# Optimization experiments

Hardware: AMD Instinct MI355X
Metric: run time of the kernel (lower is better)

Reference implementation:

```python
import jax, jax.numpy as jnp
import numpy as np

B, H, W, K, A = 4096, 32, 32, 20, 4


def setup_inputs() -> dict:
    key = jax.random.key(0)
    k_wall, k_agent, k_goal, k_phi, k_l1, k_l2 = jax.random.split(key, 6)
    # obs channels: 0 = wall/feature map (random), 1 = one-hot agent pos, 2 = one-hot goal pos
    walls = jax.random.uniform(k_wall, (B, H, W), dtype=jnp.float32)
    agent_idx = jax.random.randint(k_agent, (B,), 0, H * W)
    goal_idx = jax.random.randint(k_goal, (B,), 0, H * W)
    agent = jax.nn.one_hot(agent_idx, H * W, dtype=jnp.float32).reshape(B, H, W)
    goal = jax.nn.one_hot(goal_idx, H * W, dtype=jnp.float32).reshape(B, H, W)
    obs = jnp.stack([walls, agent, goal], axis=-1)  # (B,H,W,3)
    obs_flat = obs.reshape(B, H * W * 3)
    din = H * W * 3
    return {
        "obs_flat": obs_flat,
        "Phi_w": jax.random.normal(k_phi, (din, 2 * H * W), dtype=jnp.float32) * 0.02,
        "Phi_b": jnp.zeros((2 * H * W,), jnp.float32),
        "L1_w": jax.random.normal(k_l1, (36, 16), dtype=jnp.float32) * 0.1,
        "L1_b": jnp.zeros((16,), jnp.float32),
        "L2_w": jax.random.normal(k_l2, (16, A), dtype=jnp.float32) * 0.1,
        "L2_b": jnp.zeros((A,), jnp.float32),
    }


def _mvprop(r, p):
    # K-step value propagation: V <- max(V, r + p*(best 4-neighbor V - r))
    # p = sigmoid(...) >= 0, so max over the 4 shifted nv values equals nv of the max shift.
    def body(V, _):
        pv = jnp.pad(V, ((0, 0), (1, 1), (1, 1)))
        nbr = jnp.maximum(
            jnp.maximum(pv[:, :-2, 1:-1], pv[:, 2:, 1:-1]),   # up, down
            jnp.maximum(pv[:, 1:-1, :-2], pv[:, 1:-1, 2:]),   # left, right
        )
        return jnp.maximum(V, r + p * (nbr - r)), None
    V, _ = jax.lax.scan(body, r, None, length=K)
    return V


def reference(obs_flat, Phi_w, Phi_b, L1_w, L1_b, L2_w, L2_b):
    b = obs_flat.shape[0]
    obs = obs_flat.reshape(b, H, W, 3)
    phi = jax.nn.sigmoid(obs_flat @ Phi_w + Phi_b).reshape(b, H, W, 2)
    r, p = phi[..., 0], phi[..., 1]
    V = _mvprop(r, p)  # (b,H,W)
    obs_val = jnp.concatenate([obs, V[..., None]], axis=-1)  # (b,H,W,4)
    padded = jnp.pad(obs_val, ((0, 0), (1, 1), (1, 1), (0, 0)))
    # agent position: exactly one nonzero in channel 1 per sample -> argmax
    idx = jnp.argmax(obs[..., 1].reshape(b, -1), axis=1)
    pi, pj = idx // W, idx % W
    # 3x3 neighborhood around agent in padded grid (start = pos+1-1 = pos)
    def slice_one(ov, i, j):
        return jax.lax.dynamic_slice(ov, (i, j, 0), (3, 3, 4))
    sel = jax.vmap(slice_one)(padded, pi, pj)  # (b,3,3,4)
    h = jax.nn.relu(sel.reshape(b, 36) @ L1_w + L1_b)
    logit = h @ L2_w + L2_b
    return logit
```

## Files before the change

### kernel.cpp

```cpp
#include <hip/hip_runtime.h>
#include <hip/hip_fp16.h>

#define BATCH 4096
#define HH 32
#define WW 32
#define KPROP 20
#define NACT 4
#define DIN 3072
#define DPHI 2048
#define HWC 1024
#define KC 1024

typedef _Float16 h8_t __attribute__((ext_vector_type(8)));
typedef _Float16 h4_t __attribute__((ext_vector_type(4)));
typedef float f32x4 __attribute__((ext_vector_type(4)));

__device__ inline float sigmoidf(float x) { return 1.0f / (1.0f + __expf(-x)); }

__device__ inline float dpp_shr1(float x) {
    return __int_as_float(__builtin_amdgcn_update_dpp(
        0, __float_as_int(x), 0x111, 0xF, 0xF, true));
}
__device__ inline float dpp_shl1(float x) {
    return __int_as_float(__builtin_amdgcn_update_dpp(
        0, __float_as_int(x), 0x101, 0xF, 0xF, true));
}

__global__ __launch_bounds__(256) void prep_fused_kernel(
    const float* __restrict__ obs,
    const float* __restrict__ Phi_w,
    _Float16* __restrict__ W16,
    _Float16* __restrict__ PwT,
    _Float16* __restrict__ Pag,
    int* __restrict__ aidx, int* __restrict__ gidx)
{
    __shared__ float tile[32][33];
    if (blockIdx.x < BATCH) {
        const int t = blockIdx.x * 256 + threadIdx.x;
        const int b = t >> 8;
        const int c0 = (t & 255) * 4;
        const float* src = obs + (size_t)b * DIN + 3 * c0;
        const float4 f0 = *(const float4*)(src);
        const float4 f1 = *(const float4*)(src + 4);
        const float4 f2 = *(const float4*)(src + 8);
        h4_t w;
        w[0] = (_Float16)f0.x; w[1] = (_Float16)f0.w;
        w[2] = (_Float16)f1.z; w[3] = (_Float16)f2.y;
        *(h4_t*)(W16 + (size_t)b * KC + c0) = w;
        if (f0.y > 0.5f) aidx[b] = c0;
        if (f1.x > 0.5f) aidx[b] = c0 + 1;
        if (f1.w > 0.5f) aidx[b] = c0 + 2;
        if (f2.z > 0.5f) aidx[b] = c0 + 3;
        if (f0.z > 0.5f) gidx[b] = c0;
        if (f1.y > 0.5f) gidx[b] = c0 + 1;
        if (f2.x > 0.5f) gidx[b] = c0 + 2;
        if (f2.w > 0.5f) gidx[b] = c0 + 3;
    } else {
        const int bid = blockIdx.x - BATCH;
        const int ni = bid & 63;
        const int ci = bid >> 6;
        const int tx = threadIdx.x & 31;
        const int ty = threadIdx.x >> 5;
        #pragma unroll
        for (int s = 0; s < 4; s++) {
            const int r = ty + 8 * s;
            const int c = ci * 32 + r;
            const int n = ni * 32 + tx;
            tile[r][tx] = Phi_w[(size_t)(3 * c) * DPHI + n];
            Pag[(size_t)c * DPHI + n]         = (_Float16)Phi_w[(size_t)(3 * c + 1) * DPHI + n];
            Pag[(size_t)(HWC + c) * DPHI + n] = (_Float16)Phi_w[(size_t)(3 * c + 2) * DPHI + n];
        }
        __syncthreads();
        #pragma unroll
        for (int s = 0; s < 4; s++) {
            const int r = ty + 8 * s;
            PwT[(size_t)(ni * 32 + r) * KC + ci * 32 + tx] = (_Float16)tile[tx][r];
        }
    }
}

__global__ __launch_bounds__(256) void gemm_pre_kernel(
    const _Float16* __restrict__ A,
    const _Float16* __restrict__ Bt,
    const float* __restrict__ bias,
    _Float16* __restrict__ pre)
{
    const int tid  = threadIdx.x;
    const int lane = tid & 63;
    const int wid  = tid >> 6;
    const int m0 = blockIdx.y * 64;
    const int n0 = blockIdx.x * 256 + wid * 64;
    const int lm = lane & 15;
    const int kq = lane >> 4;

    const _Float16* Ap = A  + (size_t)(m0 + lm) * KC + kq * 8;
    const _Float16* Bp = Bt + (size_t)(n0 + lm) * KC + kq * 8;

    f32x4 acc[4][4] = {};
    h8_t a_cur[4], b_cur[4], a_nxt[4], b_nxt[4];

    #pragma unroll
    for (int i = 0; i < 4; i++) {
        a_cur[i] = *(const h8_t*)(Ap + (size_t)i * 16 * KC);
        b_cur[i] = *(const h8_t*)(Bp + (size_t)i * 16 * KC);
    }

    for (int k0 = 32; k0 <= KC; k0 += 32) {
        if (k0 < KC) {
            #pragma unroll
            for (int i = 0; i < 4; i++) {
                a_nxt[i] = *(const h8_t*)(Ap + (size_t)i * 16 * KC + k0);
                b_nxt[i] = *(const h8_t*)(Bp + (size_t)i * 16 * KC + k0);
            }
        }
        #pragma unroll
        for (int mt = 0; mt < 4; mt++)
            #pragma unroll
            for (int nt = 0; nt < 4; nt++)
                acc[mt][nt] = __builtin_amdgcn_mfma_f32_16x16x32_f16(
                    a_cur[mt], b_cur[nt], acc[mt][nt], 0, 0, 0);
        #pragma unroll
        for (int i = 0; i < 4; i++) { a_cur[i] = a_nxt[i]; b_cur[i] = b_nxt[i]; }
    }

    #pragma unroll
    for (int nt = 0; nt < 4; nt++) {
        const int col = n0 + nt * 16 + lm;
        const float bcol = bias[col];
        #pragma unroll
        for (int mt = 0; mt < 4; mt++) {
            #pragma unroll
            for (int r = 0; r < 4; r++) {
                const int row = m0 + mt * 16 + kq * 4 + r;
                pre[(size_t)row * DPHI + col] = (_Float16)(acc[mt][nt][r] + bcol);
            }
        }
    }
}

__global__ __launch_bounds__(256, 4) void vprop_head_kernel(
    const _Float16* __restrict__ pre,
    const _Float16* __restrict__ Pag,
    const float* __restrict__ obs,
    const int* __restrict__ aidx,
    const int* __restrict__ gidx,
    const float* __restrict__ L1w,
    const float* __restrict__ L1b,
    const float* __restrict__ L2w,
    const float* __restrict__ L2b,
    float* __restrict__ out)
{
    __shared__ __align__(16) float Vg[4][HWC];
    __shared__ float sel[4][36], hbuf[4][16];

    const int tid  = threadIdx.x;
    const int w    = tid >> 6;
    const int lane = tid & 63;
    const int b    = blockIdx.x * 4 + w;
    const int bi   = lane & 15;
    const int bj   = lane >> 4;
    const int ai = aidx[b];
    const int gi = gidx[b];

    const _Float16* pb = pre + (size_t)b * DPHI;
    const _Float16* ra = Pag + (size_t)ai * DPHI;
    const _Float16* rg = Pag + (size_t)(HWC + gi) * DPHI;

    float v[2][8], p[2][8], a[2][8];
    #pragma unroll
    for (int r = 0; r < 2; r++) {
        const int off = 64 * (2 * bi + r) + 16 * bj;
        const h8_t ph0 = *(const h8_t*)(pb + off), ph1 = *(const h8_t*)(pb + off + 8);
        const h8_t pa0 = *(const h8_t*)(ra + off), pa1 = *(const h8_t*)(ra + off + 8);
        const h8_t pg0 = *(const h8_t*)(rg + off), pg1 = *(const h8_t*)(rg + off + 8);
        #pragma unroll
        for (int c = 0; c < 4; c++) {
            const float rv = sigmoidf((float)ph0[2*c]   + (float)pa0[2*c]   + (float)pg0[2*c]);
            const float pv = sigmoidf((float)ph0[2*c+1] + (float)pa0[2*c+1] + (float)pg0[2*c+1]);
            v[r][c] = rv; p[r][c] = pv; a[r][c] = rv * (1.0f - pv);
            const float rv2 = sigmoidf((float)ph1[2*c]   + (float)pa1[2*c]   + (float)pg1[2*c]);
            const float pv2 = sigmoidf((float)ph1[2*c+1] + (float)pa1[2*c+1] + (float)pg1[2*c+1]);
            v[r][c+4] = rv2; p[r][c+4] = pv2; a[r][c+4] = rv2 * (1.0f - pv2);
        }
    }

    for (int it = 0; it < KPROP; it++) {
        float uh[8], dh[8], lh[2], rh[2];
        #pragma unroll
        for (int c = 0; c < 8; c++) {
            uh[c] = dpp_shr1(v[1][c]);
            dh[c] = dpp_shl1(v[0][c]);
        }
        #pragma unroll
        for (int r = 0; r < 2; r++) {
            lh[r] = __shfl(v[r][7], lane - 16);
            rh[r] = __shfl(v[r][0], lane + 16);
            if (bj == 0) lh[r] = 0.0f;
            if (bj == 3) rh[r] = 0.0f;
        }
        float nb[2][8];
        #pragma unroll
        for (int c = 0; c < 8; c++) {
            const float lf0 = (c == 0) ? lh[0] : v[0][c-1];
            const float rt0 = (c == 7) ? rh[0] : v[0][c+1];
            const float lf1 = (c == 0) ? lh[1] : v[1][c-1];
            const float rt1 = (c == 7) ? rh[1] : v[1][c+1];
            nb[0][c] = fmaxf(fmaxf(uh[c], v[1][c]), fmaxf(lf0, rt0));
            nb[1][c] = fmaxf(fmaxf(v[0][c], dh[c]), fmaxf(lf1, rt1));
        }
        #pragma unroll
        for (int r = 0; r < 2; r++)
            #pragma unroll
            for (int c = 0; c < 8; c++)
                v[r][c] = fmaxf(v[r][c], fmaf(p[r][c], nb[r][c], a[r][c]));
    }

    #pragma unroll
    for (int r = 0; r < 2; r++) {
        float4 lo, hi;
        lo.x = v[r][0]; lo.y = v[r][1]; lo.z = v[r][2]; lo.w = v[r][3];
        hi.x = v[r][4]; hi.y = v[r][5]; hi.z = v[r][6]; hi.w = v[r][7];
        const int base = (2 * bi + r) * 32 + 8 * bj;
        *(float4*)&Vg[w][base]     = lo;
        *(float4*)&Vg[w][base + 4] = hi;
    }
    __syncthreads();

    const int pi = ai >> 5, pj = ai & 31;
    if (lane < 36) {
        const int cell = lane >> 2;
        const int ch = lane & 3;
        const int di = pi + cell / 3 - 1;
        const int dj = pj + cell % 3 - 1;
        float vv = 0.0f;
        if (di >= 0 && di < HH && dj >= 0 && dj < WW) {
            const int c = di * WW + dj;
            vv = (ch < 3) ? obs[(size_t)b * DIN + 3 * c + ch] : Vg[w][c];
        }
        sel[w][lane] = vv;
    }
    __syncthreads();

    if (lane < 16) {
        float h = L1b[lane];
        #pragma unroll
        for (int k = 0; k < 36; k++) h += sel[w][k] * L1w[k * 16 + lane];
        hbuf[w][lane] = fmaxf(h, 0.0f);
    }
    __syncthreads();

    if (lane < 4) {
        float o = L2b[lane];
        #pragma unroll
        for (int t = 0; t < 16; t++) o += hbuf[w][t] * L2w[t * 4 + lane];
        out[(size_t)b * NACT + lane] = o;
    }
}

extern "C" void kernel_launch(void* const* d_in, const int* in_sizes, int n_in,
                              void* d_out, int out_size, void* d_ws, size_t ws_size,
                              hipStream_t stream) {
    const float* obs   = (const float*)d_in[0];
    const float* Phi_w = (const float*)d_in[1];
    const float* Phi_b = (const float*)d_in[2];
    const float* L1w   = (const float*)d_in[3];
    const float* L1b   = (const float*)d_in[4];
    const float* L2w   = (const float*)d_in[5];
    const float* L2b   = (const float*)d_in[6];
    float* out = (float*)d_out;

    char* ws = (char*)d_ws;
    _Float16* pre = (_Float16*)ws;
    _Float16* W16 = (_Float16*)(ws + 16777216);
    _Float16* PwT = (_Float16*)(ws + 25165824);
    _Float16* Pag = (_Float16*)(ws + 29360128);
    int* aidx = (int*)(ws + 37748736);
    int* gidx = aidx + BATCH;

    prep_fused_kernel<<<BATCH + 2048, 256, 0, stream>>>(obs, Phi_w, W16, PwT, Pag, aidx, gidx);
    gemm_pre_kernel<<<dim3(DPHI / 256, BATCH / 64), 256, 0, stream>>>(W16, PwT, Phi_b, pre);
    vprop_head_kernel<<<BATCH / 4, 256, 0, stream>>>(pre, Pag, obs, aidx, gidx,
                                                     L1w, L1b, L2w, L2b, out);
}
```

Baseline: 197.2 us.

## Pre-pack GEMM operands into MFMA fragment layout with double-buffered loads

The prep kernel now writes the fp16 A and B operands into a tiled layout where each 16-row by 8-k fragment is contiguous. Each wave can then fetch a whole MFMA fragment with one fully coalesced 1 KB load instead of 16 strided row segments. The GEMM main loop is restructured into two register buffers that alternate each half-iteration to overlap loads with MFMAs. The LDS transpose of Phi_w is removed, so B is written with scattered 2-byte stores, which may make the prep stage more expensive.

```diff
diff --git a/kernel.cpp b/kernel.cpp
--- a/kernel.cpp
+++ b/kernel.cpp
@@ -10,6 +10,7 @@
 #define DPHI 2048
 #define HWC 1024
 #define KC 1024
+#define TILE_ELEMS (16 * KC)
 
 typedef _Float16 h8_t __attribute__((ext_vector_type(8)));
 typedef _Float16 h4_t __attribute__((ext_vector_type(4)));
@@ -26,15 +27,18 @@
         0, __float_as_int(x), 0x101, 0xF, 0xF, true));
 }
 
+__device__ inline size_t pack_off(int row, int k) {
+    return (size_t)(row >> 4) * TILE_ELEMS + (k >> 3) * 128 + (row & 15) * 8 + (k & 7);
+}
+
 __global__ __launch_bounds__(256) void prep_fused_kernel(
     const float* __restrict__ obs,
     const float* __restrict__ Phi_w,
-    _Float16* __restrict__ W16,
-    _Float16* __restrict__ PwT,
+    _Float16* __restrict__ A_pack,
+    _Float16* __restrict__ B_pack,
     _Float16* __restrict__ Pag,
     int* __restrict__ aidx, int* __restrict__ gidx)
 {
-    __shared__ float tile[32][33];
     if (blockIdx.x < BATCH) {
         const int t = blockIdx.x * 256 + threadIdx.x;
         const int b = t >> 8;
@@ -46,7 +50,7 @@
         h4_t w;
         w[0] = (_Float16)f0.x; w[1] = (_Float16)f0.w;
         w[2] = (_Float16)f1.z; w[3] = (_Float16)f2.y;
-        *(h4_t*)(W16 + (size_t)b * KC + c0) = w;
+        *(h4_t*)(A_pack + pack_off(b, c0)) = w;
         if (f0.y > 0.5f) aidx[b] = c0;
         if (f1.x > 0.5f) aidx[b] = c0 + 1;
         if (f1.w > 0.5f) aidx[b] = c0 + 2;
@@ -66,22 +70,17 @@
             const int r = ty + 8 * s;
             const int c = ci * 32 + r;
             const int n = ni * 32 + tx;
-            tile[r][tx] = Phi_w[(size_t)(3 * c) * DPHI + n];
+            const float w0 = Phi_w[(size_t)(3 * c) * DPHI + n];
             Pag[(size_t)c * DPHI + n]         = (_Float16)Phi_w[(size_t)(3 * c + 1) * DPHI + n];
             Pag[(size_t)(HWC + c) * DPHI + n] = (_Float16)Phi_w[(size_t)(3 * c + 2) * DPHI + n];
-        }
-        __syncthreads();
-        #pragma unroll
-        for (int s = 0; s < 4; s++) {
-            const int r = ty + 8 * s;
-            PwT[(size_t)(ni * 32 + r) * KC + ci * 32 + tx] = (_Float16)tile[tx][r];
+            B_pack[pack_off(n, c)] = (_Float16)w0;
         }
     }
 }
 
 __global__ __launch_bounds__(256) void gemm_pre_kernel(
-    const _Float16* __restrict__ A,
-    const _Float16* __restrict__ Bt,
+    const _Float16* __restrict__ A_pack,
+    const _Float16* __restrict__ B_pack,
     const float* __restrict__ bias,
     _Float16* __restrict__ pre)
 {
@@ -93,34 +92,47 @@
     const int lm = lane & 15;
     const int kq = lane >> 4;
 
-    const _Float16* Ap = A  + (size_t)(m0 + lm) * KC + kq * 8;
-    const _Float16* Bp = Bt + (size_t)(n0 + lm) * KC + kq * 8;
+    const _Float16* Abase = A_pack + (size_t)(blockIdx.y * 4) * TILE_ELEMS + 8 * lane;
+    const _Float16* Bbase = B_pack + (size_t)(blockIdx.x * 16 + wid * 4) * TILE_ELEMS + 8 * lane;
 
     f32x4 acc[4][4] = {};
-    h8_t a_cur[4], b_cur[4], a_nxt[4], b_nxt[4];
+    h8_t a0[4], b0[4], a1[4], b1[4];
 
     #pragma unroll
     for (int i = 0; i < 4; i++) {
-        a_cur[i] = *(const h8_t*)(Ap + (size_t)i * 16 * KC);
-        b_cur[i] = *(const h8_t*)(Bp + (size_t)i * 16 * KC);
-    }
-
-    for (int k0 = 32; k0 <= KC; k0 += 32) {
-        if (k0 < KC) {
-            #pragma unroll
-            for (int i = 0; i < 4; i++) {
-                a_nxt[i] = *(const h8_t*)(Ap + (size_t)i * 16 * KC + k0);
-                b_nxt[i] = *(const h8_t*)(Bp + (size_t)i * 16 * KC + k0);
-            }
-        }
+        a0[i] = *(const h8_t*)(Abase + i * TILE_ELEMS);
+        b0[i] = *(const h8_t*)(Bbase + i * TILE_ELEMS);
+        a1[i] = *(const h8_t*)(Abase + i * TILE_ELEMS + 32 * 16);
+        b1[i] = *(const h8_t*)(Bbase + i * TILE_ELEMS + 32 * 16);
+    }
+
+    for (int k0 = 0; k0 < KC; k0 += 64) {
         #pragma unroll
         for (int mt = 0; mt < 4; mt++)
             #pragma unroll
             for (int nt = 0; nt < 4; nt++)
                 acc[mt][nt] = __builtin_amdgcn_mfma_f32_16x16x32_f16(
-                    a_cur[mt], b_cur[nt], acc[mt][nt], 0, 0, 0);
-        #pragma unroll
-        for (int i = 0; i < 4; i++) { a_cur[i] = a_nxt[i]; b_cur[i] = b_nxt[i]; }
+                    a0[mt], b0[nt], acc[mt][nt], 0, 0, 0);
+        if (k0 + 64 < KC) {
+            #pragma unroll
+            for (int i = 0; i < 4; i++) {
+                a0[i] = *(const h8_t*)(Abase + i * TILE_ELEMS + (k0 + 64) * 16);
+                b0[i] = *(const h8_t*)(Bbase + i * TILE_ELEMS + (k0 + 64) * 16);
+            }
+        }
+        #pragma unroll
+        for (int mt = 0; mt < 4; mt++)
+            #pragma unroll
+            for (int nt = 0; nt < 4; nt++)
+                acc[mt][nt] = __builtin_amdgcn_mfma_f32_16x16x32_f16(
+                    a1[mt], b1[nt], acc[mt][nt], 0, 0, 0);
+        if (k0 + 96 < KC) {
+            #pragma unroll
+            for (int i = 0; i < 4; i++) {
+                a1[i] = *(const h8_t*)(Abase + i * TILE_ELEMS + (k0 + 96) * 16);
+                b1[i] = *(const h8_t*)(Bbase + i * TILE_ELEMS + (k0 + 96) * 16);
+            }
+        }
     }
 
     #pragma unroll
@@ -270,15 +282,15 @@
     float* out = (float*)d_out;
 
     char* ws = (char*)d_ws;
-    _Float16* pre = (_Float16*)ws;
-    _Float16* W16 = (_Float16*)(ws + 16777216);
-    _Float16* PwT = (_Float16*)(ws + 25165824);
-    _Float16* Pag = (_Float16*)(ws + 29360128);
+    _Float16* pre    = (_Float16*)ws;
+    _Float16* A_pack = (_Float16*)(ws + 16777216);
+    _Float16* B_pack = (_Float16*)(ws + 25165824);
+    _Float16* Pag    = (_Float16*)(ws + 29360128);
     int* aidx = (int*)(ws + 37748736);
     int* gidx = aidx + BATCH;
 
-    prep_fused_kernel<<<BATCH + 2048, 256, 0, stream>>>(obs, Phi_w, W16, PwT, Pag, aidx, gidx);
-    gemm_pre_kernel<<<dim3(DPHI / 256, BATCH / 64), 256, 0, stream>>>(W16, PwT, Phi_b, pre);
+    prep_fused_kernel<<<BATCH + 2048, 256, 0, stream>>>(obs, Phi_w, A_pack, B_pack, Pag, aidx, gidx);
+    gemm_pre_kernel<<<dim3(DPHI / 256, BATCH / 64), 256, 0, stream>>>(A_pack, B_pack, Phi_b, pre);
     vprop_head_kernel<<<BATCH / 4, 256, 0, stream>>>(pre, Pag, obs, aidx, gidx,
                                                      L1w, L1b, L2w, L2b, out);
 }
```

New measurement: 163.9 us. -16.9%, faster.
